# Performance work log

Hardware: AMD Instinct MI355X
Metric: run time of the kernel (lower is better)

The kernel has to match this reference:

```python
import jax, jax.numpy as jnp
import numpy as np

DIM = 256

def _feat(x):
    # ELU(x) + 1 feature map (positive features for linear attention)
    return jax.nn.elu(x) + 1.0

def setup_inputs() -> dict:
    key = jax.random.key(0)
    ks = jax.random.split(key, 9)
    B, L, D = 8, 4096, DIM
    s = 1.0 / np.sqrt(D)
    return {
        'q': jax.random.normal(ks[0], (B, L, D), jnp.float32),
        'k': jax.random.normal(ks[1], (B, L, D), jnp.float32),
        'v': jax.random.normal(ks[2], (B, L, D), jnp.float32),
        'Wq': jax.random.normal(ks[3], (D, D), jnp.float32) * s,
        'bq': jnp.zeros((D,), jnp.float32),
        'Wk': jax.random.normal(ks[4], (D, D), jnp.float32) * s,
        'bk': jnp.zeros((D,), jnp.float32),
        'Wv': jax.random.normal(ks[5], (D, D), jnp.float32) * s,
        'bv': jnp.zeros((D,), jnp.float32),
    }

def reference(q, k, v, Wq, bq, Wk, bk, Wv, bv):
    Q = _feat(q @ Wq + bq)              # [B,L,D]
    K = _feat(k @ Wk + bk)              # [B,L,D]
    V = v @ Wv + bv                     # [B,L,D]
    kv = jnp.einsum('bld,blh->bdh', K, V)          # [B,D,D] summary
    z = jnp.einsum('bld,bd->bl', Q, K.sum(axis=1)) + 1e-6  # [B,L]
    out = jnp.einsum('bld,bdh->blh', Q, kv)        # [B,L,D]
    return out / z[..., None]
```

## Files before the change

kernel.cpp:

```cpp
#include <hip/hip_runtime.h>
#include <hip/hip_bf16.h>

#define DIM 256
#define BATCH 8
#define SEQ 4096
#define MTOT (BATCH*SEQ)
#define NSPLIT 8

typedef __attribute__((ext_vector_type(8))) short bf16x8;
typedef __attribute__((ext_vector_type(4))) float f32x4;
typedef __attribute__((ext_vector_type(8))) unsigned short u16x8;
typedef __attribute__((ext_vector_type(4))) unsigned short u16x4;

__device__ inline unsigned short f2b(float f){
  unsigned int u = __float_as_uint(f);
  u = u + 0x7FFFu + ((u >> 16) & 1u);
  return (unsigned short)(u >> 16);
}
__device__ inline float b2f(unsigned short h){
  return __uint_as_float(((unsigned int)h) << 16);
}


template<bool F32>
__device__ inline void load_half(const void* src, int ld, int h, int tid,
                                 f32x4* vf, u16x8* vh){
  int row = tid >> 1, c0 = h*128 + (tid & 1)*64;
  if constexpr (F32){
    const float* p = (const float*)src + (long)row*ld + c0;
    #pragma unroll
    for (int j = 0; j < 16; j++) vf[j] = *(const f32x4*)(p + 4*j);
  } else {
    const unsigned short* p = (const unsigned short*)src + (long)row*ld + c0;
    #pragma unroll
    for (int j = 0; j < 8; j++) vh[j] = *(const u16x8*)(p + 8*j);
  }
}

template<bool F32>
__device__ inline void write_half(const f32x4* vf, const u16x8* vh, int tid,
                                  unsigned short* lds){
  unsigned short tmp[64];
  if constexpr (F32){
    #pragma unroll
    for (int j = 0; j < 16; j++){
      f32x4 f = vf[j];
      tmp[4*j+0] = f2b(f[0]); tmp[4*j+1] = f2b(f[1]);
      tmp[4*j+2] = f2b(f[2]); tmp[4*j+3] = f2b(f[3]);
    }
  } else {
    #pragma unroll
    for (int j = 0; j < 8; j++) *(u16x8*)&tmp[8*j] = vh[j];
  }
  int row = tid >> 1, sw = (row & 7) << 4;
  char* rb = (char*)lds + row*256 + (tid & 1)*128;
  #pragma unroll
  for (int j = 0; j < 8; j++)
    *(u16x8*)(rb + ((j*16) ^ sw)) = *(const u16x8*)&tmp[8*j];
}

__device__ inline void mma_half(const unsigned short* lA, const unsigned short* lB,
                                int lane, int wr, int wc, f32x4 acc[4][4]){
  int r0 = lane & 15, kg16 = (lane >> 4) * 16;
  #pragma unroll
  for (int ksub = 0; ksub < 4; ksub++){
    int kb = ksub*64 + kg16;
    bf16x8 af[4], bf[4];
    #pragma unroll
    for (int m = 0; m < 4; m++){
      int row = wr*64 + m*16 + r0;
      af[m] = *(const bf16x8*)((const char*)lA + row*256 + (kb ^ ((row & 7) << 4)));
    }
    #pragma unroll
    for (int n = 0; n < 4; n++){
      int row = wc*64 + n*16 + r0;
      bf[n] = *(const bf16x8*)((const char*)lB + row*256 + (kb ^ ((row & 7) << 4)));
    }
    #pragma unroll
    for (int m = 0; m < 4; m++)
      #pragma unroll
      for (int n = 0; n < 4; n++)
        acc[m][n] = __builtin_amdgcn_mfma_f32_16x16x32_bf16(af[m], bf[n], acc[m][n], 0, 0, 0);
  }
}

template<bool AF32, bool BF32>
__device__ inline void gemm256(const void* A, int lda, const void* B, int ldb,
                               int tid, int lane, int wr, int wc,
                               unsigned short* lA, unsigned short* lB,
                               f32x4 acc[4][4]){
  f32x4 a0f[16], a1f[16], b0f[16], b1f[16];
  u16x8 a0h[8], a1h[8], b0h[8], b1h[8];
  load_half<AF32>(A, lda, 0, tid, a0f, a0h);
  load_half<BF32>(B, ldb, 0, tid, b0f, b0h);
  __syncthreads();
  write_half<AF32>(a0f, a0h, tid, lA);
  write_half<BF32>(b0f, b0h, tid, lB);
  load_half<AF32>(A, lda, 1, tid, a1f, a1h);
  load_half<BF32>(B, ldb, 1, tid, b1f, b1h);
  __syncthreads();
  mma_half(lA, lB, lane, wr, wc, acc);
  __syncthreads();
  write_half<AF32>(a1f, a1h, tid, lA);
  write_half<BF32>(b1f, b1h, tid, lB);
  __syncthreads();
  mma_half(lA, lB, lane, wr, wc, acc);
}

__global__ __launch_bounds__(256) void prep_wt(const float* __restrict__ Wq, const float* __restrict__ Wk,
                                               const float* __restrict__ Wv, unsigned short* __restrict__ Wt){
  int i = blockIdx.x*256 + threadIdx.x;
  int s = i >> 16, r = i & 65535, n = r & 255, kk = r >> 8;
  const float* W = (s == 0) ? Wq : ((s == 1) ? Wk : Wv);
  Wt[s*65536 + n*256 + kk] = f2b(W[kk*256 + n]);
}

__global__ __launch_bounds__(256) void proj_all_ker(const float* __restrict__ qin, const float* __restrict__ kin,
                                                    const float* __restrict__ vin,
                                                    const unsigned short* __restrict__ Wt,
                                                    const float* __restrict__ bqp, const float* __restrict__ bkp,
                                                    const float* __restrict__ bvp,
                                                    unsigned short* __restrict__ Qo,
                                                    unsigned short* __restrict__ Kt, unsigned short* __restrict__ Vt,
                                                    float* __restrict__ ksum){
  __shared__ unsigned short lA[128*128], lB[128*128];
  int lt = blockIdx.x, dt = blockIdx.y;
  int bz = blockIdx.z, sel = bz % 3, b = bz / 3;
  int tid = threadIdx.x, lane = tid & 63, w = tid >> 6, wr = w >> 1, wc = w & 1;

  const float* X = (sel == 0 ? kin : (sel == 1 ? vin : qin)) + ((long)b*SEQ + (long)lt*128)*DIM;
  const unsigned short* Wb = Wt + ((sel + 1) % 3)*DIM*DIM + dt*128*DIM;
  const float* bias = (sel == 0 ? bkp : (sel == 1 ? bvp : bqp));

  f32x4 acc[4][4] = {};
  if (sel == 2) gemm256<true , false>(X , DIM, Wb, DIM, tid, lane, wr, wc, lA, lB, acc);
  else          gemm256<false, true >(Wb, DIM, X , DIM, tid, lane, wr, wc, lA, lB, acc);

  int r0 = lane & 15, rg = lane >> 4;

  if (sel == 2){
    #pragma unroll
    for (int n = 0; n < 4; n++){
      int col = dt*128 + wc*64 + n*16 + r0;
      float bv = bias[col];
      #pragma unroll
      for (int m = 0; m < 4; m++)
        #pragma unroll
        for (int r = 0; r < 4; r++){
          long row = (long)b*SEQ + lt*128 + wr*64 + m*16 + rg*4 + r;
          float vv = acc[m][n][r] + bv;
          vv = vv > 0.f ? vv + 1.f : expf(vv);
          Qo[row*DIM + col] = f2b(vv);
        }
    }
    return;
  }

  unsigned short* Yt = (sel == 1 ? Vt : Kt) + (long)b*DIM*SEQ;
  float sums[4][4];
  #pragma unroll
  for (int m = 0; m < 4; m++) for (int r = 0; r < 4; r++) sums[m][r] = 0.f;
  #pragma unroll
  for (int m = 0; m < 4; m++)
    #pragma unroll
    for (int r = 0; r < 4; r++){
      int row = dt*128 + wr*64 + m*16 + rg*4 + r;
      float bvv = bias[row];
      #pragma unroll
      for (int n = 0; n < 4; n++){
        int col = lt*128 + wc*64 + n*16 + r0;
        float vv = acc[m][n][r] + bvv;
        if (sel == 0) vv = vv > 0.f ? vv + 1.f : expf(vv);
        Yt[(long)row*SEQ + col] = f2b(vv);
        sums[m][r] += vv;
      }
    }
  if (sel == 0){
    #pragma unroll
    for (int m = 0; m < 4; m++)
      #pragma unroll
      for (int r = 0; r < 4; r++){
        float s = sums[m][r];
        s += __shfl_xor(s, 1); s += __shfl_xor(s, 2);
        s += __shfl_xor(s, 4); s += __shfl_xor(s, 8);
        if (r0 == 0){
          int row = dt*128 + wr*64 + m*16 + rg*4 + r;
          atomicAdd(&ksum[b*DIM + row], s);
        }
      }
  }
}

__global__ __launch_bounds__(256) void kv_ker(const unsigned short* __restrict__ Vt, const unsigned short* __restrict__ Kt,
                                              float* __restrict__ kvp){
  __shared__ unsigned short lA[128*128], lB[128*128];
  int qd = blockIdx.x, mt = qd >> 1, nt = qd & 1;
  int ksp = blockIdx.y, b = blockIdx.z;
  int tid = threadIdx.x, lane = tid & 63, w = tid >> 6, wr = w >> 1, wc = w & 1;
  const unsigned short* A = Vt + (long)b*DIM*SEQ + (long)mt*128*SEQ + ksp*512;
  const unsigned short* B = Kt + (long)b*DIM*SEQ + (long)nt*128*SEQ + ksp*512;
  f32x4 acc[4][4] = {};
  gemm256<false,false>(A      , SEQ, B      , SEQ, tid, lane, wr, wc, lA, lB, acc);
  gemm256<false,false>(A + 256, SEQ, B + 256, SEQ, tid, lane, wr, wc, lA, lB, acc);
  int r0 = lane & 15, rg = lane >> 4;
  float* base = kvp + (long)(ksp*BATCH + b)*DIM*DIM;
  #pragma unroll
  for (int m = 0; m < 4; m++)
    #pragma unroll
    for (int n = 0; n < 4; n++)
      #pragma unroll
      for (int r = 0; r < 4; r++){
        int row = mt*128 + wr*64 + m*16 + rg*4 + r;
        int col = nt*128 + wc*64 + n*16 + r0;
        base[row*DIM + col] = acc[m][n][r];
      }
}

__global__ __launch_bounds__(256) void kv_reduce(const float* __restrict__ kvp, unsigned short* __restrict__ kvb){
  int i = blockIdx.x*256 + threadIdx.x;
  int b = i >> 16, e = i & 65535;
  float s = 0.f;
  #pragma unroll
  for (int sp = 0; sp < NSPLIT; sp++) s += kvp[(long)(sp*BATCH + b)*65536 + e];
  kvb[i] = f2b(s);
}

__global__ __launch_bounds__(256) void zker(const unsigned short* __restrict__ Q, const float* __restrict__ ksum,
                                            float* __restrict__ z){
  int g = blockIdx.x*4 + (threadIdx.x >> 6);
  int lane = threadIdx.x & 63;
  int b = g >> 12;
  u16x4 qv = *(const u16x4*)(Q + (long)g*DIM + lane*4);
  const float* kp = ksum + b*DIM + lane*4;
  float s = b2f(qv[0])*kp[0] + b2f(qv[1])*kp[1] + b2f(qv[2])*kp[2] + b2f(qv[3])*kp[3];
  #pragma unroll
  for (int o = 1; o < 64; o <<= 1) s += __shfl_xor(s, o);
  if (lane == 0) z[g] = s + 1e-6f;
}

__global__ __launch_bounds__(256) void out_ker(const unsigned short* __restrict__ Q, const unsigned short* __restrict__ kvb,
                                               const float* __restrict__ z, float* __restrict__ out){
  __shared__ unsigned short lA[128*128], lB[128*128];
  int lt = blockIdx.x, ht = blockIdx.y, b = blockIdx.z;
  int tid = threadIdx.x, lane = tid & 63, w = tid >> 6, wr = w >> 1, wc = w & 1;
  const unsigned short* A = Q + ((long)b*SEQ + (long)lt*128)*DIM;
  const unsigned short* B = kvb + b*DIM*DIM + ht*128*DIM;
  f32x4 acc[4][4] = {};
  gemm256<false,false>(A, DIM, B, DIM, tid, lane, wr, wc, lA, lB, acc);
  int r0 = lane & 15, rg = lane >> 4;
  #pragma unroll
  for (int m = 0; m < 4; m++)
    #pragma unroll
    for (int r = 0; r < 4; r++){
      long g = (long)b*SEQ + lt*128 + wr*64 + m*16 + rg*4 + r;
      float inv = 1.0f / z[g];
      #pragma unroll
      for (int n = 0; n < 4; n++){
        int col = ht*128 + wc*64 + n*16 + r0;
        out[g*DIM + col] = acc[m][n][r] * inv;
      }
    }
}

extern "C" void kernel_launch(void* const* d_in, const int* in_sizes, int n_in,
                              void* d_out, int out_size, void* d_ws, size_t ws_size,
                              hipStream_t stream){
  const float* q  = (const float*)d_in[0];
  const float* k  = (const float*)d_in[1];
  const float* v  = (const float*)d_in[2];
  const float* Wq = (const float*)d_in[3];
  const float* bq = (const float*)d_in[4];
  const float* Wk = (const float*)d_in[5];
  const float* bk = (const float*)d_in[6];
  const float* Wv = (const float*)d_in[7];
  const float* bv = (const float*)d_in[8];
  float* out = (float*)d_out;

  char* ws = (char*)d_ws;
  size_t off = 0;
  auto alloc = [&](size_t bytes){ void* p = ws + off; off += (bytes + 255) & ~(size_t)255; return p; };
  unsigned short* Q   = (unsigned short*)alloc((size_t)MTOT*DIM*2);
  unsigned short* Kt  = (unsigned short*)alloc((size_t)BATCH*DIM*SEQ*2);
  unsigned short* Vt  = (unsigned short*)alloc((size_t)BATCH*DIM*SEQ*2);
  unsigned short* Wt  = (unsigned short*)alloc((size_t)3*DIM*DIM*2);
  float*          kvp = (float*)alloc((size_t)NSPLIT*BATCH*DIM*DIM*4);
  unsigned short* kvb = (unsigned short*)alloc((size_t)BATCH*DIM*DIM*2);
  float*          ksum= (float*)alloc((size_t)BATCH*DIM*4);
  float*          zb  = (float*)alloc((size_t)MTOT*4);

  hipMemsetAsync(ksum, 0, (size_t)BATCH*DIM*4, stream);

  hipLaunchKernelGGL(prep_wt,     dim3(768),        dim3(256), 0, stream, Wq, Wk, Wv, Wt);
  hipLaunchKernelGGL(proj_all_ker,dim3(32,2,24),    dim3(256), 0, stream, q, k, v, Wt, bq, bk, bv, Q, Kt, Vt, ksum);
  hipLaunchKernelGGL(kv_ker,      dim3(4,NSPLIT,8), dim3(256), 0, stream, Vt, Kt, kvp);
  hipLaunchKernelGGL(kv_reduce,   dim3(2048),       dim3(256), 0, stream, kvp, kvb);
  hipLaunchKernelGGL(zker,        dim3(8192),       dim3(256), 0, stream, Q, ksum, zb);
  hipLaunchKernelGGL(out_ker,     dim3(32,2,8),     dim3(256), 0, stream, Q, kvb, zb, out);
}
```

Baseline: 235.5 us.

## Load MFMA fragments directly from global memory instead of staging through LDS

Removes the shared-memory staging (load_half/write_half/mma_half) from the projection, kv and output GEMM kernels. Each wave now reads its bf16 (or fp32, converted on the fly) MFMA fragments straight from global memory. This drops the LDS writes and block barriers, and frees LDS so more blocks can be resident per CU. The cost is that fragments shared between waves are fetched redundantly through the caches, with narrow strided accesses, and fp32 inputs are reconverted by every wave that uses them.

```diff
diff --git a/kernel.cpp b/kernel.cpp
--- a/kernel.cpp
+++ b/kernel.cpp
@@ -21,90 +21,19 @@
   return __uint_as_float(((unsigned int)h) << 16);
 }
 
-
-template<bool F32>
-__device__ inline void load_half(const void* src, int ld, int h, int tid,
-                                 f32x4* vf, u16x8* vh){
-  int row = tid >> 1, c0 = h*128 + (tid & 1)*64;
-  if constexpr (F32){
-    const float* p = (const float*)src + (long)row*ld + c0;
-    #pragma unroll
-    for (int j = 0; j < 16; j++) vf[j] = *(const f32x4*)(p + 4*j);
-  } else {
-    const unsigned short* p = (const unsigned short*)src + (long)row*ld + c0;
-    #pragma unroll
-    for (int j = 0; j < 8; j++) vh[j] = *(const u16x8*)(p + 8*j);
-  }
-}
-
-template<bool F32>
-__device__ inline void write_half(const f32x4* vf, const u16x8* vh, int tid,
-                                  unsigned short* lds){
-  unsigned short tmp[64];
-  if constexpr (F32){
-    #pragma unroll
-    for (int j = 0; j < 16; j++){
-      f32x4 f = vf[j];
-      tmp[4*j+0] = f2b(f[0]); tmp[4*j+1] = f2b(f[1]);
-      tmp[4*j+2] = f2b(f[2]); tmp[4*j+3] = f2b(f[3]);
-    }
-  } else {
-    #pragma unroll
-    for (int j = 0; j < 8; j++) *(u16x8*)&tmp[8*j] = vh[j];
-  }
-  int row = tid >> 1, sw = (row & 7) << 4;
-  char* rb = (char*)lds + row*256 + (tid & 1)*128;
-  #pragma unroll
-  for (int j = 0; j < 8; j++)
-    *(u16x8*)(rb + ((j*16) ^ sw)) = *(const u16x8*)&tmp[8*j];
-}
-
-__device__ inline void mma_half(const unsigned short* lA, const unsigned short* lB,
-                                int lane, int wr, int wc, f32x4 acc[4][4]){
-  int r0 = lane & 15, kg16 = (lane >> 4) * 16;
-  #pragma unroll
-  for (int ksub = 0; ksub < 4; ksub++){
-    int kb = ksub*64 + kg16;
-    bf16x8 af[4], bf[4];
-    #pragma unroll
-    for (int m = 0; m < 4; m++){
-      int row = wr*64 + m*16 + r0;
-      af[m] = *(const bf16x8*)((const char*)lA + row*256 + (kb ^ ((row & 7) << 4)));
-    }
-    #pragma unroll
-    for (int n = 0; n < 4; n++){
-      int row = wc*64 + n*16 + r0;
-      bf[n] = *(const bf16x8*)((const char*)lB + row*256 + (kb ^ ((row & 7) << 4)));
-    }
-    #pragma unroll
-    for (int m = 0; m < 4; m++)
-      #pragma unroll
-      for (int n = 0; n < 4; n++)
-        acc[m][n] = __builtin_amdgcn_mfma_f32_16x16x32_bf16(af[m], bf[n], acc[m][n], 0, 0, 0);
-  }
-}
-
-template<bool AF32, bool BF32>
-__device__ inline void gemm256(const void* A, int lda, const void* B, int ldb,
-                               int tid, int lane, int wr, int wc,
-                               unsigned short* lA, unsigned short* lB,
-                               f32x4 acc[4][4]){
-  f32x4 a0f[16], a1f[16], b0f[16], b1f[16];
-  u16x8 a0h[8], a1h[8], b0h[8], b1h[8];
-  load_half<AF32>(A, lda, 0, tid, a0f, a0h);
-  load_half<BF32>(B, ldb, 0, tid, b0f, b0h);
-  __syncthreads();
-  write_half<AF32>(a0f, a0h, tid, lA);
-  write_half<BF32>(b0f, b0h, tid, lB);
-  load_half<AF32>(A, lda, 1, tid, a1f, a1h);
-  load_half<BF32>(B, ldb, 1, tid, b1f, b1h);
-  __syncthreads();
-  mma_half(lA, lB, lane, wr, wc, acc);
-  __syncthreads();
-  write_half<AF32>(a1f, a1h, tid, lA);
-  write_half<BF32>(b1f, b1h, tid, lB);
-  __syncthreads();
-  mma_half(lA, lB, lane, wr, wc, acc);
+__device__ inline bf16x8 ldfrag_b(const unsigned short* base, long row0, int ld, int k0, int lane){
+  return *(const bf16x8*)(base + (row0 + (lane & 15))*(long)ld + k0 + ((lane >> 4) << 3));
+}
+__device__ inline bf16x8 ldfrag_f(const float* base, long row0, int ld, int k0, int lane){
+  const float* p = base + (row0 + (lane & 15))*(long)ld + k0 + ((lane >> 4) << 3);
+  f32x4 lo = *(const f32x4*)p;
+  f32x4 hi = *(const f32x4*)(p + 4);
+  bf16x8 r;
+  r[0] = (short)f2b(lo[0]); r[1] = (short)f2b(lo[1]);
+  r[2] = (short)f2b(lo[2]); r[3] = (short)f2b(lo[3]);
+  r[4] = (short)f2b(hi[0]); r[5] = (short)f2b(hi[1]);
+  r[6] = (short)f2b(hi[2]); r[7] = (short)f2b(hi[3]);
+  return r;
 }
 
 __global__ __launch_bounds__(256) void prep_wt(const float* __restrict__ Wq, const float* __restrict__ Wk,
@@ -123,7 +52,6 @@
                                                     unsigned short* __restrict__ Qo,
                                                     unsigned short* __restrict__ Kt, unsigned short* __restrict__ Vt,
                                                     float* __restrict__ ksum){
-  __shared__ unsigned short lA[128*128], lB[128*128];
   int lt = blockIdx.x, dt = blockIdx.y;
   int bz = blockIdx.z, sel = bz % 3, b = bz / 3;
   int tid = threadIdx.x, lane = tid & 63, w = tid >> 6, wr = w >> 1, wc = w & 1;
@@ -133,8 +61,37 @@
   const float* bias = (sel == 0 ? bkp : (sel == 1 ? bvp : bqp));
 
   f32x4 acc[4][4] = {};
-  if (sel == 2) gemm256<true , false>(X , DIM, Wb, DIM, tid, lane, wr, wc, lA, lB, acc);
-  else          gemm256<false, true >(Wb, DIM, X , DIM, tid, lane, wr, wc, lA, lB, acc);
+  if (sel == 2){
+    #pragma unroll
+    for (int ks = 0; ks < 8; ks++){
+      int k0 = ks*32;
+      bf16x8 af[4], bf[4];
+      #pragma unroll
+      for (int m = 0; m < 4; m++) af[m] = ldfrag_f(X , wr*64 + m*16, DIM, k0, lane);
+      #pragma unroll
+      for (int n = 0; n < 4; n++) bf[n] = ldfrag_b(Wb, wc*64 + n*16, DIM, k0, lane);
+      #pragma unroll
+      for (int m = 0; m < 4; m++)
+        #pragma unroll
+        for (int n = 0; n < 4; n++)
+          acc[m][n] = __builtin_amdgcn_mfma_f32_16x16x32_bf16(af[m], bf[n], acc[m][n], 0, 0, 0);
+    }
+  } else {
+    #pragma unroll
+    for (int ks = 0; ks < 8; ks++){
+      int k0 = ks*32;
+      bf16x8 af[4], bf[4];
+      #pragma unroll
+      for (int m = 0; m < 4; m++) af[m] = ldfrag_b(Wb, wr*64 + m*16, DIM, k0, lane);
+      #pragma unroll
+      for (int n = 0; n < 4; n++) bf[n] = ldfrag_f(X , wc*64 + n*16, DIM, k0, lane);
+      #pragma unroll
+      for (int m = 0; m < 4; m++)
+        #pragma unroll
+        for (int n = 0; n < 4; n++)
+          acc[m][n] = __builtin_amdgcn_mfma_f32_16x16x32_bf16(af[m], bf[n], acc[m][n], 0, 0, 0);
+    }
+  }
 
   int r0 = lane & 15, rg = lane >> 4;
 
@@ -193,15 +150,27 @@
 
 __global__ __launch_bounds__(256) void kv_ker(const unsigned short* __restrict__ Vt, const unsigned short* __restrict__ Kt,
                                               float* __restrict__ kvp){
-  __shared__ unsigned short lA[128*128], lB[128*128];
   int qd = blockIdx.x, mt = qd >> 1, nt = qd & 1;
   int ksp = blockIdx.y, b = blockIdx.z;
   int tid = threadIdx.x, lane = tid & 63, w = tid >> 6, wr = w >> 1, wc = w & 1;
-  const unsigned short* A = Vt + (long)b*DIM*SEQ + (long)mt*128*SEQ + ksp*512;
-  const unsigned short* B = Kt + (long)b*DIM*SEQ + (long)nt*128*SEQ + ksp*512;
+  const unsigned short* A = Vt + (long)b*DIM*SEQ + (long)mt*128*SEQ;
+  const unsigned short* B = Kt + (long)b*DIM*SEQ + (long)nt*128*SEQ;
+  int l0 = ksp*(SEQ/NSPLIT);
   f32x4 acc[4][4] = {};
-  gemm256<false,false>(A      , SEQ, B      , SEQ, tid, lane, wr, wc, lA, lB, acc);
-  gemm256<false,false>(A + 256, SEQ, B + 256, SEQ, tid, lane, wr, wc, lA, lB, acc);
+  #pragma unroll 4
+  for (int ks = 0; ks < (SEQ/NSPLIT)/32; ks++){
+    int k0 = l0 + ks*32;
+    bf16x8 af[4], bf[4];
+    #pragma unroll
+    for (int m = 0; m < 4; m++) af[m] = ldfrag_b(A, wr*64 + m*16, SEQ, k0, lane);
+    #pragma unroll
+    for (int n = 0; n < 4; n++) bf[n] = ldfrag_b(B, wc*64 + n*16, SEQ, k0, lane);
+    #pragma unroll
+    for (int m = 0; m < 4; m++)
+      #pragma unroll
+      for (int n = 0; n < 4; n++)
+        acc[m][n] = __builtin_amdgcn_mfma_f32_16x16x32_bf16(af[m], bf[n], acc[m][n], 0, 0, 0);
+  }
   int r0 = lane & 15, rg = lane >> 4;
   float* base = kvp + (long)(ksp*BATCH + b)*DIM*DIM;
   #pragma unroll
@@ -240,13 +209,25 @@
 
 __global__ __launch_bounds__(256) void out_ker(const unsigned short* __restrict__ Q, const unsigned short* __restrict__ kvb,
                                                const float* __restrict__ z, float* __restrict__ out){
-  __shared__ unsigned short lA[128*128], lB[128*128];
   int lt = blockIdx.x, ht = blockIdx.y, b = blockIdx.z;
   int tid = threadIdx.x, lane = tid & 63, w = tid >> 6, wr = w >> 1, wc = w & 1;
   const unsigned short* A = Q + ((long)b*SEQ + (long)lt*128)*DIM;
   const unsigned short* B = kvb + b*DIM*DIM + ht*128*DIM;
   f32x4 acc[4][4] = {};
-  gemm256<false,false>(A, DIM, B, DIM, tid, lane, wr, wc, lA, lB, acc);
+  #pragma unroll
+  for (int ks = 0; ks < 8; ks++){
+    int k0 = ks*32;
+    bf16x8 af[4], bf[4];
+    #pragma unroll
+    for (int m = 0; m < 4; m++) af[m] = ldfrag_b(A, wr*64 + m*16, DIM, k0, lane);
+    #pragma unroll
+    for (int n = 0; n < 4; n++) bf[n] = ldfrag_b(B, wc*64 + n*16, DIM, k0, lane);
+    #pragma unroll
+    for (int m = 0; m < 4; m++)
+      #pragma unroll
+      for (int n = 0; n < 4; n++)
+        acc[m][n] = __builtin_amdgcn_mfma_f32_16x16x32_bf16(af[m], bf[n], acc[m][n], 0, 0, 0);
+  }
   int r0 = lane & 15, rg = lane >> 4;
   #pragma unroll
   for (int m = 0; m < 4; m++)
```

After: 279.1 us. +18.5%, slower.

## Stage GEMM tiles with direct global-to-LDS loads and smaller tiles

Applied to the files above, without the earlier changes.

Replaces the register-staged GEMM tile loader with __builtin_amdgcn_global_load_lds direct copies into swizzled LDS. fp32 activations are now converted to bf16 when fragments are read from LDS rather than before the store. The loop runs over 64-wide k chunks with 128x64 output tiles, which doubles grid sizes and cuts LDS per block so more blocks fit per CU. The combined projection kernel is split into separate K/V and Q kernels, and their epilogues now transpose through LDS so global stores are coalesced. In exchange, each k step has its own sync pair with no double buffering, and fp32 tiles double the LDS read traffic.

```diff
diff --git a/kernel.cpp b/kernel.cpp
--- a/kernel.cpp
+++ b/kernel.cpp
@@ -1,5 +1,6 @@
 #include <hip/hip_runtime.h>
 #include <hip/hip_bf16.h>
+#include <math.h>
 
 #define DIM 256
 #define BATCH 8
@@ -21,90 +22,76 @@
   return __uint_as_float(((unsigned int)h) << 16);
 }
 
-
-template<bool F32>
-__device__ inline void load_half(const void* src, int ld, int h, int tid,
-                                 f32x4* vf, u16x8* vh){
-  int row = tid >> 1, c0 = h*128 + (tid & 1)*64;
-  if constexpr (F32){
-    const float* p = (const float*)src + (long)row*ld + c0;
-    #pragma unroll
-    for (int j = 0; j < 16; j++) vf[j] = *(const f32x4*)(p + 4*j);
-  } else {
-    const unsigned short* p = (const unsigned short*)src + (long)row*ld + c0;
-    #pragma unroll
-    for (int j = 0; j < 8; j++) vh[j] = *(const u16x8*)(p + 8*j);
-  }
-}
-
-template<bool F32>
-__device__ inline void write_half(const f32x4* vf, const u16x8* vh, int tid,
-                                  unsigned short* lds){
-  unsigned short tmp[64];
-  if constexpr (F32){
-    #pragma unroll
-    for (int j = 0; j < 16; j++){
-      f32x4 f = vf[j];
-      tmp[4*j+0] = f2b(f[0]); tmp[4*j+1] = f2b(f[1]);
-      tmp[4*j+2] = f2b(f[2]); tmp[4*j+3] = f2b(f[3]);
-    }
-  } else {
-    #pragma unroll
-    for (int j = 0; j < 8; j++) *(u16x8*)&tmp[8*j] = vh[j];
-  }
-  int row = tid >> 1, sw = (row & 7) << 4;
-  char* rb = (char*)lds + row*256 + (tid & 1)*128;
-  #pragma unroll
-  for (int j = 0; j < 8; j++)
-    *(u16x8*)(rb + ((j*16) ^ sw)) = *(const u16x8*)&tmp[8*j];
-}
-
-__device__ inline void mma_half(const unsigned short* lA, const unsigned short* lB,
-                                int lane, int wr, int wc, f32x4 acc[4][4]){
-  int r0 = lane & 15, kg16 = (lane >> 4) * 16;
-  #pragma unroll
-  for (int ksub = 0; ksub < 4; ksub++){
-    int kb = ksub*64 + kg16;
-    bf16x8 af[4], bf[4];
+__device__ __forceinline__ void gl2lds16(const void* g, void* l){
+  __builtin_amdgcn_global_load_lds(
+      (const __attribute__((address_space(1))) void*)g,
+      (__attribute__((address_space(3))) void*)l, 16, 0, 0);
+}
+
+template<int R>
+__device__ __forceinline__ void stage_b16(const unsigned short* g, int ld, void* lds, int tid){
+  int lane = tid & 63;
+  #pragma unroll
+  for (int i = 0; i < R/32; i++){
+    int c = (tid >> 6)*(R/32) + i;
+    int row = c*8 + (lane >> 3);
+    int s = lane & 7;
+    gl2lds16((const char*)(g + (long)row*ld) + ((s ^ (row & 7)) << 4),
+             (char*)lds + c*1024);
+  }
+}
+template<int R>
+__device__ __forceinline__ void stage_f32(const float* g, int ld, void* lds, int tid){
+  int lane = tid & 63;
+  #pragma unroll
+  for (int i = 0; i < R/16; i++){
+    int c = (tid >> 6)*(R/16) + i;
+    int row = c*4 + (lane >> 4);
+    int s = lane & 15;
+    gl2lds16((const char*)(g + (long)row*ld) + ((s ^ (row & 15)) << 4),
+             (char*)lds + c*1024);
+  }
+}
+
+__device__ __forceinline__ bf16x8 rdfrag_b(const void* lds, int row0, int kk, int lane){
+  int row = row0 + (lane & 15);
+  int s = (kk*4 + (lane >> 4)) ^ (row & 7);
+  return *(const bf16x8*)((const char*)lds + row*128 + s*16);
+}
+__device__ __forceinline__ bf16x8 rdfrag_f(const void* lds, int row0, int kk, int lane){
+  int row = row0 + (lane & 15);
+  int s0 = kk*8 + ((lane >> 4) << 1);
+  const char* rp = (const char*)lds + row*256;
+  f32x4 lo = *(const f32x4*)(rp + ((s0       ^ (row & 15)) << 4));
+  f32x4 hi = *(const f32x4*)(rp + (((s0 + 1) ^ (row & 15)) << 4));
+  bf16x8 r;
+  r[0]=(short)f2b(lo[0]); r[1]=(short)f2b(lo[1]); r[2]=(short)f2b(lo[2]); r[3]=(short)f2b(lo[3]);
+  r[4]=(short)f2b(hi[0]); r[5]=(short)f2b(hi[1]); r[6]=(short)f2b(hi[2]); r[7]=(short)f2b(hi[3]);
+  return r;
+}
+
+template<bool AF32, bool BF32>
+__device__ __forceinline__ void mma64(const void* lA, const void* lB, int lane,
+                                      int wr, int wc, f32x4 acc[4][2]){
+  #pragma unroll
+  for (int kk = 0; kk < 2; kk++){
+    bf16x8 af[4], bf[2];
     #pragma unroll
     for (int m = 0; m < 4; m++){
-      int row = wr*64 + m*16 + r0;
-      af[m] = *(const bf16x8*)((const char*)lA + row*256 + (kb ^ ((row & 7) << 4)));
-    }
-    #pragma unroll
-    for (int n = 0; n < 4; n++){
-      int row = wc*64 + n*16 + r0;
-      bf[n] = *(const bf16x8*)((const char*)lB + row*256 + (kb ^ ((row & 7) << 4)));
+      if constexpr (AF32) af[m] = rdfrag_f(lA, wr*64 + m*16, kk, lane);
+      else                af[m] = rdfrag_b(lA, wr*64 + m*16, kk, lane);
+    }
+    #pragma unroll
+    for (int n = 0; n < 2; n++){
+      if constexpr (BF32) bf[n] = rdfrag_f(lB, wc*32 + n*16, kk, lane);
+      else                bf[n] = rdfrag_b(lB, wc*32 + n*16, kk, lane);
     }
     #pragma unroll
     for (int m = 0; m < 4; m++)
       #pragma unroll
-      for (int n = 0; n < 4; n++)
+      for (int n = 0; n < 2; n++)
         acc[m][n] = __builtin_amdgcn_mfma_f32_16x16x32_bf16(af[m], bf[n], acc[m][n], 0, 0, 0);
   }
-}
-
-template<bool AF32, bool BF32>
-__device__ inline void gemm256(const void* A, int lda, const void* B, int ldb,
-                               int tid, int lane, int wr, int wc,
-                               unsigned short* lA, unsigned short* lB,
-                               f32x4 acc[4][4]){
-  f32x4 a0f[16], a1f[16], b0f[16], b1f[16];
-  u16x8 a0h[8], a1h[8], b0h[8], b1h[8];
-  load_half<AF32>(A, lda, 0, tid, a0f, a0h);
-  load_half<BF32>(B, ldb, 0, tid, b0f, b0h);
-  __syncthreads();
-  write_half<AF32>(a0f, a0h, tid, lA);
-  write_half<BF32>(b0f, b0h, tid, lB);
-  load_half<AF32>(A, lda, 1, tid, a1f, a1h);
-  load_half<BF32>(B, ldb, 1, tid, b1f, b1h);
-  __syncthreads();
-  mma_half(lA, lB, lane, wr, wc, acc);
-  __syncthreads();
-  write_half<AF32>(a1f, a1h, tid, lA);
-  write_half<BF32>(b1f, b1h, tid, lB);
-  __syncthreads();
-  mma_half(lA, lB, lane, wr, wc, acc);
 }
 
 __global__ __launch_bounds__(256) void prep_wt(const float* __restrict__ Wq, const float* __restrict__ Wk,
@@ -115,67 +102,60 @@
   Wt[s*65536 + n*256 + kk] = f2b(W[kk*256 + n]);
 }
 
-__global__ __launch_bounds__(256) void proj_all_ker(const float* __restrict__ qin, const float* __restrict__ kin,
-                                                    const float* __restrict__ vin,
-                                                    const unsigned short* __restrict__ Wt,
-                                                    const float* __restrict__ bqp, const float* __restrict__ bkp,
-                                                    const float* __restrict__ bvp,
-                                                    unsigned short* __restrict__ Qo,
-                                                    unsigned short* __restrict__ Kt, unsigned short* __restrict__ Vt,
-                                                    float* __restrict__ ksum){
-  __shared__ unsigned short lA[128*128], lB[128*128];
+__global__ __launch_bounds__(256) void proj_kv_ker(const float* __restrict__ kin, const float* __restrict__ vin,
+                                                   const unsigned short* __restrict__ Wt,
+                                                   const float* __restrict__ bkp, const float* __restrict__ bvp,
+                                                   unsigned short* __restrict__ Kt, unsigned short* __restrict__ Vt,
+                                                   float* __restrict__ ksum){
+  __shared__ __align__(1024) char smem[32*1024];
   int lt = blockIdx.x, dt = blockIdx.y;
-  int bz = blockIdx.z, sel = bz % 3, b = bz / 3;
+  int z = blockIdx.z, sv = z & 1, b = z >> 1;
   int tid = threadIdx.x, lane = tid & 63, w = tid >> 6, wr = w >> 1, wc = w & 1;
-
-  const float* X = (sel == 0 ? kin : (sel == 1 ? vin : qin)) + ((long)b*SEQ + (long)lt*128)*DIM;
-  const unsigned short* Wb = Wt + ((sel + 1) % 3)*DIM*DIM + dt*128*DIM;
-  const float* bias = (sel == 0 ? bkp : (sel == 1 ? bvp : bqp));
-
-  f32x4 acc[4][4] = {};
-  if (sel == 2) gemm256<true , false>(X , DIM, Wb, DIM, tid, lane, wr, wc, lA, lB, acc);
-  else          gemm256<false, true >(Wb, DIM, X , DIM, tid, lane, wr, wc, lA, lB, acc);
+  const float* X = (sv ? vin : kin) + ((long)b*SEQ + (long)lt*64)*DIM;
+  const unsigned short* Wb = Wt + (sv ? 2 : 1)*65536 + dt*128*256;
+  const float* bias = sv ? bvp : bkp;
+  void* lA = smem; void* lB = smem + 16*1024;
+
+  f32x4 acc[4][2] = {};
+  for (int kt = 0; kt < 4; kt++){
+    __syncthreads();
+    stage_b16<128>(Wb + kt*64, 256, lA, tid);
+    stage_f32<64>(X + kt*64, DIM, lB, tid);
+    __syncthreads();
+    mma64<false, true>(lA, lB, lane, wr, wc, acc);
+  }
 
   int r0 = lane & 15, rg = lane >> 4;
-
-  if (sel == 2){
-    #pragma unroll
-    for (int n = 0; n < 4; n++){
-      int col = dt*128 + wc*64 + n*16 + r0;
-      float bv = bias[col];
-      #pragma unroll
-      for (int m = 0; m < 4; m++)
-        #pragma unroll
-        for (int r = 0; r < 4; r++){
-          long row = (long)b*SEQ + lt*128 + wr*64 + m*16 + rg*4 + r;
-          float vv = acc[m][n][r] + bv;
-          vv = vv > 0.f ? vv + 1.f : expf(vv);
-          Qo[row*DIM + col] = f2b(vv);
-        }
-    }
-    return;
-  }
-
-  unsigned short* Yt = (sel == 1 ? Vt : Kt) + (long)b*DIM*SEQ;
+  unsigned short* ldsT = (unsigned short*)smem;
   float sums[4][4];
   #pragma unroll
   for (int m = 0; m < 4; m++) for (int r = 0; r < 4; r++) sums[m][r] = 0.f;
+  __syncthreads();
   #pragma unroll
   for (int m = 0; m < 4; m++)
     #pragma unroll
     for (int r = 0; r < 4; r++){
-      int row = dt*128 + wr*64 + m*16 + rg*4 + r;
-      float bvv = bias[row];
-      #pragma unroll
-      for (int n = 0; n < 4; n++){
-        int col = lt*128 + wc*64 + n*16 + r0;
+      int dl = wr*64 + m*16 + rg*4 + r;
+      float bvv = bias[dt*128 + dl];
+      #pragma unroll
+      for (int n = 0; n < 2; n++){
+        int ll = wc*32 + n*16 + r0;
         float vv = acc[m][n][r] + bvv;
-        if (sel == 0) vv = vv > 0.f ? vv + 1.f : expf(vv);
-        Yt[(long)row*SEQ + col] = f2b(vv);
+        if (!sv) vv = vv > 0.f ? vv + 1.f : expf(vv);
+        ldsT[dl*64 + ll] = f2b(vv);
         sums[m][r] += vv;
       }
     }
-  if (sel == 0){
+  __syncthreads();
+  unsigned short* Yt = (sv ? Vt : Kt) + (long)b*DIM*SEQ;
+  {
+    int row = tid >> 1, hf = tid & 1;
+    const unsigned short* sp = ldsT + row*64 + hf*32;
+    unsigned short* dp = Yt + (long)(dt*128 + row)*SEQ + lt*64 + hf*32;
+    #pragma unroll
+    for (int j = 0; j < 4; j++) *(u16x8*)(dp + j*8) = *(const u16x8*)(sp + j*8);
+  }
+  if (!sv){
     #pragma unroll
     for (int m = 0; m < 4; m++)
       #pragma unroll
@@ -184,36 +164,91 @@
         s += __shfl_xor(s, 1); s += __shfl_xor(s, 2);
         s += __shfl_xor(s, 4); s += __shfl_xor(s, 8);
         if (r0 == 0){
-          int row = dt*128 + wr*64 + m*16 + rg*4 + r;
-          atomicAdd(&ksum[b*DIM + row], s);
+          int dl = wr*64 + m*16 + rg*4 + r;
+          atomicAdd(&ksum[b*DIM + dt*128 + dl], s);
         }
       }
+  }
+}
+
+__global__ __launch_bounds__(256) void proj_q_ker(const float* __restrict__ qin,
+                                                  const unsigned short* __restrict__ Wt,
+                                                  const float* __restrict__ bqp,
+                                                  unsigned short* __restrict__ Qo){
+  __shared__ __align__(1024) char smem[40*1024];
+  int lt = blockIdx.x, dt = blockIdx.y, b = blockIdx.z;
+  int tid = threadIdx.x, lane = tid & 63, w = tid >> 6, wr = w >> 1, wc = w & 1;
+  const float* X = qin + ((long)b*SEQ + (long)lt*128)*DIM;
+  const unsigned short* Wb = Wt + dt*64*256;
+  void* lA = smem; void* lB = smem + 32*1024;
+
+  f32x4 acc[4][2] = {};
+  for (int kt = 0; kt < 4; kt++){
+    __syncthreads();
+    stage_f32<128>(X + kt*64, DIM, lA, tid);
+    stage_b16<64>(Wb + kt*64, 256, lB, tid);
+    __syncthreads();
+    mma64<true, false>(lA, lB, lane, wr, wc, acc);
+  }
+
+  int r0 = lane & 15, rg = lane >> 4;
+  unsigned short* ldsT = (unsigned short*)smem;
+  __syncthreads();
+  #pragma unroll
+  for (int n = 0; n < 2; n++){
+    int dl = wc*32 + n*16 + r0;
+    float bvv = bqp[dt*64 + dl];
+    #pragma unroll
+    for (int m = 0; m < 4; m++)
+      #pragma unroll
+      for (int r = 0; r < 4; r++){
+        int ll = wr*64 + m*16 + rg*4 + r;
+        float vv = acc[m][n][r] + bvv;
+        vv = vv > 0.f ? vv + 1.f : expf(vv);
+        ldsT[ll*64 + dl] = f2b(vv);
+      }
+  }
+  __syncthreads();
+  {
+    int row = tid >> 1, hf = tid & 1;
+    const unsigned short* sp = ldsT + row*64 + hf*32;
+    unsigned short* dp = Qo + ((long)b*SEQ + lt*128 + row)*DIM + dt*64 + hf*32;
+    #pragma unroll
+    for (int j = 0; j < 4; j++) *(u16x8*)(dp + j*8) = *(const u16x8*)(sp + j*8);
   }
 }
 
 __global__ __launch_bounds__(256) void kv_ker(const unsigned short* __restrict__ Vt, const unsigned short* __restrict__ Kt,
                                               float* __restrict__ kvp){
-  __shared__ unsigned short lA[128*128], lB[128*128];
-  int qd = blockIdx.x, mt = qd >> 1, nt = qd & 1;
+  __shared__ __align__(1024) char smem[24*1024];
+  int x = blockIdx.x, mt = x >> 2, nt = x & 3;
   int ksp = blockIdx.y, b = blockIdx.z;
   int tid = threadIdx.x, lane = tid & 63, w = tid >> 6, wr = w >> 1, wc = w & 1;
   const unsigned short* A = Vt + (long)b*DIM*SEQ + (long)mt*128*SEQ + ksp*512;
-  const unsigned short* B = Kt + (long)b*DIM*SEQ + (long)nt*128*SEQ + ksp*512;
-  f32x4 acc[4][4] = {};
-  gemm256<false,false>(A      , SEQ, B      , SEQ, tid, lane, wr, wc, lA, lB, acc);
-  gemm256<false,false>(A + 256, SEQ, B + 256, SEQ, tid, lane, wr, wc, lA, lB, acc);
+  const unsigned short* B = Kt + (long)b*DIM*SEQ + (long)nt*64*SEQ  + ksp*512;
+  void* lA = smem; void* lB = smem + 16*1024;
+
+  f32x4 acc[4][2] = {};
+  for (int kt = 0; kt < 8; kt++){
+    __syncthreads();
+    stage_b16<128>(A + kt*64, SEQ, lA, tid);
+    stage_b16<64>(B + kt*64, SEQ, lB, tid);
+    __syncthreads();
+    mma64<false, false>(lA, lB, lane, wr, wc, acc);
+  }
   int r0 = lane & 15, rg = lane >> 4;
   float* base = kvp + (long)(ksp*BATCH + b)*DIM*DIM;
   #pragma unroll
   for (int m = 0; m < 4; m++)
     #pragma unroll
-    for (int n = 0; n < 4; n++)
-      #pragma unroll
-      for (int r = 0; r < 4; r++){
-        int row = mt*128 + wr*64 + m*16 + rg*4 + r;
-        int col = nt*128 + wc*64 + n*16 + r0;
-        base[row*DIM + col] = acc[m][n][r];
-      }
+    for (int r = 0; r < 4; r++){
+      int h = mt*128 + wr*64 + m*16 + rg*4 + r;
+      #pragma unroll
+      for (int n = 0; n < 2; n++){
+        int d = nt*64 + wc*32 + n*16 + r0;
+        base[h*DIM + d] = acc[m][n][r];
+      }
+    }
 }
 
 __global__ __launch_bounds__(256) void kv_reduce(const float* __restrict__ kvp, unsigned short* __restrict__ kvb){
@@ -240,13 +275,21 @@
 
 __global__ __launch_bounds__(256) void out_ker(const unsigned short* __restrict__ Q, const unsigned short* __restrict__ kvb,
                                                const float* __restrict__ z, float* __restrict__ out){
-  __shared__ unsigned short lA[128*128], lB[128*128];
+  __shared__ __align__(1024) char smem[24*1024];
   int lt = blockIdx.x, ht = blockIdx.y, b = blockIdx.z;
   int tid = threadIdx.x, lane = tid & 63, w = tid >> 6, wr = w >> 1, wc = w & 1;
   const unsigned short* A = Q + ((long)b*SEQ + (long)lt*128)*DIM;
-  const unsigned short* B = kvb + b*DIM*DIM + ht*128*DIM;
-  f32x4 acc[4][4] = {};
-  gemm256<false,false>(A, DIM, B, DIM, tid, lane, wr, wc, lA, lB, acc);
+  const unsigned short* B = kvb + b*65536 + ht*64*DIM;
+  void* lA = smem; void* lB = smem + 16*1024;
+
+  f32x4 acc[4][2] = {};
+  for (int kt = 0; kt < 4; kt++){
+    __syncthreads();
+    stage_b16<128>(A + kt*64, DIM, lA, tid);
+    stage_b16<64>(B + kt*64, DIM, lB, tid);
+    __syncthreads();
+    mma64<false, false>(lA, lB, lane, wr, wc, acc);
+  }
   int r0 = lane & 15, rg = lane >> 4;
   #pragma unroll
   for (int m = 0; m < 4; m++)
@@ -255,8 +298,8 @@
       long g = (long)b*SEQ + lt*128 + wr*64 + m*16 + rg*4 + r;
       float inv = 1.0f / z[g];
       #pragma unroll
-      for (int n = 0; n < 4; n++){
-        int col = ht*128 + wc*64 + n*16 + r0;
+      for (int n = 0; n < 2; n++){
+        int col = ht*64 + wc*32 + n*16 + r0;
         out[g*DIM + col] = acc[m][n][r] * inv;
       }
     }
@@ -290,10 +333,11 @@
 
   hipMemsetAsync(ksum, 0, (size_t)BATCH*DIM*4, stream);
 
-  hipLaunchKernelGGL(prep_wt,     dim3(768),        dim3(256), 0, stream, Wq, Wk, Wv, Wt);
-  hipLaunchKernelGGL(proj_all_ker,dim3(32,2,24),    dim3(256), 0, stream, q, k, v, Wt, bq, bk, bv, Q, Kt, Vt, ksum);
-  hipLaunchKernelGGL(kv_ker,      dim3(4,NSPLIT,8), dim3(256), 0, stream, Vt, Kt, kvp);
-  hipLaunchKernelGGL(kv_reduce,   dim3(2048),       dim3(256), 0, stream, kvp, kvb);
-  hipLaunchKernelGGL(zker,        dim3(8192),       dim3(256), 0, stream, Q, ksum, zb);
-  hipLaunchKernelGGL(out_ker,     dim3(32,2,8),     dim3(256), 0, stream, Q, kvb, zb, out);
-}
+  hipLaunchKernelGGL(prep_wt,    dim3(768),      dim3(256), 0, stream, Wq, Wk, Wv, Wt);
+  hipLaunchKernelGGL(proj_kv_ker,dim3(64,2,16),  dim3(256), 0, stream, k, v, Wt, bk, bv, Kt, Vt, ksum);
+  hipLaunchKernelGGL(proj_q_ker, dim3(32,4,8),   dim3(256), 0, stream, q, Wt, bq, Q);
+  hipLaunchKernelGGL(kv_ker,     dim3(8,NSPLIT,8),dim3(256), 0, stream, Vt, Kt, kvp);
+  hipLaunchKernelGGL(kv_reduce,  dim3(2048),     dim3(256), 0, stream, kvp, kvb);
+  hipLaunchKernelGGL(zker,       dim3(8192),     dim3(256), 0, stream, Q, ksum, zb);
+  hipLaunchKernelGGL(out_ker,    dim3(32,4,8),   dim3(256), 0, stream, Q, kvb, zb, out);
+}
```

After: 249.8 us. 1.06x slower.
